# Kernel optimization log

Hardware: AMD Instinct MI355X
Metric: run time of the kernel (lower is better)

Reference implementation:

```python
import jax, jax.numpy as jnp
import numpy as np

NUM_BASES = 5
STRIDE = (1, 1)
PADDING = ((1, 1), (1, 1))
DN = ('NCHW', 'OIHW', 'NCHW')


def quantize_act(x):
    # Q_A_DOREFA forward: round(clamp(x, 0, 1)) -> values in {0, 1}
    return jnp.round(jnp.clip(x, 0.0, 1.0))


def quantize_w(w):
    # Q_W forward: sign(w) * mean(|w|) over the whole weight tensor of one basis
    return jnp.sign(w) * jnp.mean(jnp.abs(w))


def setup_inputs() -> dict:
    key = jax.random.key(0)
    kx, kw = jax.random.split(key)
    x = jax.random.normal(kx, (8, 256, 64, 64), dtype=jnp.float32)
    # 5 bases, each an OIHW conv kernel [256, 256, 3, 3]
    weights = jax.random.normal(kw, (NUM_BASES, 256, 256, 3, 3), dtype=jnp.float32) * 0.05
    return {"x": x, "weights": weights}


def reference(x, weights):
    xq = quantize_act(x)
    # quantize each basis independently (per-basis scalar scale)
    wq = jax.vmap(quantize_w)(weights)  # [5, O, I, kh, kw]
    # conv is linear in the kernel: sum of 5 convs == conv with summed kernels
    w_sum = jnp.sum(wq, axis=0)
    out = jax.lax.conv_general_dilated(
        xq, w_sum, window_strides=STRIDE, padding=PADDING,
        dimension_numbers=DN)
    return out / NUM_BASES
```

## Files before the change

kernel.cpp:

```cpp
#include <hip/hip_runtime.h>
#include <hip/hip_bf16.h>

typedef __attribute__((ext_vector_type(4))) int i32x4;

constexpr int NB = 8, CI = 256, OC = 256, HH = 64, WW = 64, HP = 66, WP = 66;
constexpr int NBASES = 5;
constexpr int WELEMS = OC * CI * 9;
constexpr int NT = 36;

__global__ void k_abs_partial(const float* __restrict__ w, float* __restrict__ part) {
    int b = blockIdx.x >> 6, chunk = blockIdx.x & 63;
    const float4* v = (const float4*)(w + (size_t)b * WELEMS + (size_t)chunk * (WELEMS / 64));
    float s = 0.f;
    for (int i = threadIdx.x; i < WELEMS / 64 / 4; i += 256) {
        float4 t = v[i];
        s += fabsf(t.x) + fabsf(t.y) + fabsf(t.z) + fabsf(t.w);
    }
    #pragma unroll
    for (int off = 32; off; off >>= 1) s += __shfl_down(s, off, 64);
    __shared__ float ls[4];
    int lane = threadIdx.x & 63, wid = threadIdx.x >> 6;
    if (lane == 0) ls[wid] = s;
    __syncthreads();
    if (threadIdx.x == 0) part[blockIdx.x] = ls[0] + ls[1] + ls[2] + ls[3];
}

__global__ void k_prep(const float* __restrict__ w, const float* __restrict__ part,
                       signed char* __restrict__ wsum8, float* __restrict__ scl,
                       const float* __restrict__ x, signed char* __restrict__ xq) {
    __shared__ float sLDS[NBASES];
    int tid = threadIdx.x;

    if (blockIdx.x < OC) {
        if (tid < 64) {
            #pragma unroll
            for (int b = 0; b < NBASES; ++b) {
                float v = part[b * 64 + tid];
                #pragma unroll
                for (int off = 32; off; off >>= 1) v += __shfl_down(v, off, 64);
                if (tid == 0) sLDS[b] = v * (1.0f / (float)WELEMS);
            }
        }
        __syncthreads();
        float sc[NBASES];
        #pragma unroll
        for (int b = 0; b < NBASES; ++b) sc[b] = sLDS[b];
        float sSum = sc[0] + sc[1] + sc[2] + sc[3] + sc[4];
        float invS = 127.0f / sSum;
        if (blockIdx.x == 0 && tid == 0)
            scl[0] = sSum * (0.2f / 127.0f);

        int o = blockIdx.x, i = tid;
        const float* base = w + ((size_t)(o * CI + i)) * 9;
        float acc[9];
        #pragma unroll
        for (int t = 0; t < 9; ++t) acc[t] = 0.f;
        #pragma unroll
        for (int b = 0; b < NBASES; ++b) {
            const float* wb = base + (size_t)b * WELEMS;
            #pragma unroll
            for (int t = 0; t < 9; ++t) {
                float xv = wb[t];
                acc[t] += (xv > 0.f) ? sc[b] : ((xv < 0.f) ? -sc[b] : 0.f);
            }
        }
        #pragma unroll
        for (int t = 0; t < 9; ++t)
            wsum8[(t * OC + o) * CI + i] = (signed char)__float2int_rn(acc[t] * invS);
        return;
    }

    int nh = blockIdx.x - OC, n = nh >> 6, h = nh & 63;
    const float* xb = x + ((size_t)n * CI) * (HH * WW) + h * WW;
    signed char* ob = xq + ((size_t)(n * HP + (h + 1)) * WP + 1) * CI;
    int w4 = tid >> 2;
    int cl = tid & 3;
    #pragma unroll
    for (int p = 0; p < 4; ++p) {
        int c = (p * 4 + cl) * 16;
        signed char pk[16];
        #pragma unroll
        for (int i = 0; i < 16; ++i) {
            float v = xb[(size_t)(c + i) * (HH * WW) + w4];
            pk[i] = (signed char)rintf(fminf(fmaxf(v, 0.f), 1.f));
        }
        *(int4*)(ob + w4 * CI + c) = *(const int4*)pk;
    }
    (ob - CI)[tid] = 0;
    (ob + 64 * CI)[tid] = 0;
    if (h == 0) {
        signed char* r0 = xq + ((size_t)(n * HP + 0) * WP) * CI;
        int4 z = {0, 0, 0, 0};
        for (int i = tid; i < WP * CI / 16; i += 256) *(int4*)(r0 + i * 16) = z;
    }
    if (h == HH - 1) {
        signed char* r65 = xq + ((size_t)(n * HP + (HP - 1)) * WP) * CI;
        int4 z = {0, 0, 0, 0};
        for (int i = tid; i < WP * CI / 16; i += 256) *(int4*)(r65 + i * 16) = z;
    }
}

__launch_bounds__(256, 2)
__global__ void k_conv(const signed char* __restrict__ xq,
                       const signed char* __restrict__ wsum,
                       const float* __restrict__ scl,
                       float* __restrict__ out) {
    __shared__ __align__(16) signed char lA[4][128 * 64];
    __shared__ __align__(16) signed char lB[4][128 * 64];

    float so = scl[0];

    int bid = blockIdx.x;
    int bx = ((bid & 7) << 6) | (bid >> 3);
    int pt = bx >> 1, ot = bx & 1;
    int pb = pt * 128;
    int n = pb >> 12;
    int h0 = (pb >> 6) & 63;
    int oc0 = ot * 128;
    int tid = threadIdx.x;

    int base0 = (n * HP + h0) * WP * CI;
    int bBase0 = oc0 * CI;

    int aOff[2], bOff[2];
    #pragma unroll
    for (int k = 0; k < 2; ++k) {
        int c = tid + k * 256;
        int row = c >> 2, sp = c & 3;
        int l = sp ^ ((row >> 1) & 3);
        aOff[k] = ((row >> 6) * WP + (row & 63)) * CI + l * 16;
        bOff[k] = row * CI + l * 16;
    }

    int lane = tid & 63, wid = tid >> 6;
    int wm = wid >> 1, wn = wid & 1;
    int g = lane >> 4, r16 = lane & 15;
    int fA[4], fB[4];
    #pragma unroll
    for (int q = 0; q < 4; ++q) {
        int ra = wm * 64 + q * 16 + r16;
        fA[q] = ra * 64 + (g ^ ((ra >> 1) & 3)) * 16;
        int rb = wn * 64 + q * 16 + r16;
        fB[q] = rb * 64 + (g ^ ((rb >> 1) & 3)) * 16;
    }

    i32x4 acc[4][4] = {};

    auto stage = [&](int t) {
        int buf = t & 3;
        int tap = t >> 2;
        int c0 = (t & 3) << 6;
        int kh = (tap * 171) >> 9;
        int kw = tap - kh * 3;
        const signed char* aSrc = xq + base0 + (kh * WP + kw) * CI + c0;
        const signed char* bSrc = wsum + tap * (OC * CI) + bBase0 + c0;
        #pragma unroll
        for (int k = 0; k < 2; ++k) {
            __builtin_amdgcn_global_load_lds(
                (const __attribute__((address_space(1))) void*)(aSrc + aOff[k]),
                (__attribute__((address_space(3))) void*)(&lA[buf][(tid + k * 256) * 16]), 16, 0, 0);
            __builtin_amdgcn_global_load_lds(
                (const __attribute__((address_space(1))) void*)(bSrc + bOff[k]),
                (__attribute__((address_space(3))) void*)(&lB[buf][(tid + k * 256) * 16]), 16, 0, 0);
        }
    };
    auto readFrags = [&](int buf, i32x4 (&aR)[4], i32x4 (&bR)[4]) {
        #pragma unroll
        for (int q = 0; q < 4; ++q) aR[q] = *(const i32x4*)&lA[buf][fA[q]];
        #pragma unroll
        for (int q = 0; q < 4; ++q) bR[q] = *(const i32x4*)&lB[buf][fB[q]];
    };
    auto mfmaCluster = [&](i32x4 (&aR)[4], i32x4 (&bR)[4]) {
        __builtin_amdgcn_s_setprio(1);
        #pragma unroll
        for (int mq = 0; mq < 4; ++mq)
            #pragma unroll
            for (int nq = 0; nq < 4; ++nq)
                acc[mq][nq] = __builtin_amdgcn_mfma_i32_16x16x64_i8(
                    aR[mq], bR[nq], acc[mq][nq], 0, 0, 0);
        __builtin_amdgcn_s_setprio(0);
    };

    stage(0); stage(1); stage(2);
    asm volatile("s_waitcnt vmcnt(8)" ::: "memory");
    __builtin_amdgcn_s_barrier();
    i32x4 a0[4], b0[4], a1[4], b1[4];
    readFrags(0, a0, b0);

    #pragma unroll 1
    for (int p = 0; p < NT / 2; ++p) {
        int t = 2 * p;
        {
            if (t + 2 <= NT - 1) asm volatile("s_waitcnt vmcnt(4)" ::: "memory");
            else                 asm volatile("s_waitcnt vmcnt(0)" ::: "memory");
            __builtin_amdgcn_s_barrier();
            __builtin_amdgcn_sched_barrier(0);
            if (t + 3 < NT) stage(t + 3);
            readFrags((t + 1) & 3, a1, b1);
            __builtin_amdgcn_sched_barrier(0);
            mfmaCluster(a0, b0);
        }
        t = 2 * p + 1;
        {
            if (t < NT - 1) {
                if (t + 2 <= NT - 1) asm volatile("s_waitcnt vmcnt(4)" ::: "memory");
                else                 asm volatile("s_waitcnt vmcnt(0)" ::: "memory");
                __builtin_amdgcn_s_barrier();
                __builtin_amdgcn_sched_barrier(0);
                if (t + 3 < NT) stage(t + 3);
                readFrags((t + 1) & 3, a0, b0);
                __builtin_amdgcn_sched_barrier(0);
            }
            mfmaCluster(a1, b1);
        }
    }

    int hw0 = pb & 4095;
    #pragma unroll
    for (int mq = 0; mq < 4; ++mq) {
        int pl = wm * 64 + mq * 16 + g * 4;
        #pragma unroll
        for (int nq = 0; nq < 4; ++nq) {
            int oc = oc0 + wn * 64 + nq * 16 + r16;
            float4 v;
            v.x = (float)acc[mq][nq][0] * so;
            v.y = (float)acc[mq][nq][1] * so;
            v.z = (float)acc[mq][nq][2] * so;
            v.w = (float)acc[mq][nq][3] * so;
            *(float4*)(out + ((size_t)(n * OC + oc) << 12) + hw0 + pl) = v;
        }
    }
}

extern "C" void kernel_launch(void* const* d_in, const int* in_sizes, int n_in,
                              void* d_out, int out_size, void* d_ws, size_t ws_size,
                              hipStream_t stream) {
    (void)in_sizes; (void)n_in; (void)out_size; (void)ws_size;
    const float* x   = (const float*)d_in[0];
    const float* wts = (const float*)d_in[1];
    float* out = (float*)d_out;
    char* wsb = (char*)d_ws;
    float* part          = (float*)wsb;
    float* scl           = (float*)(wsb + 2048);
    signed char* wsum8   = (signed char*)(wsb + 4096);
    signed char* xq8     = (signed char*)(wsb + (size_t)(2u << 20));

    hipLaunchKernelGGL(k_abs_partial, dim3(NBASES * 64), dim3(256), 0, stream, wts, part);
    hipLaunchKernelGGL(k_prep, dim3(OC + NB * HH), dim3(256), 0, stream,
                       wts, part, wsum8, scl, x, xq8);
    hipLaunchKernelGGL(k_conv, dim3((NB * HH * WW / 128) * (OC / 128)), dim3(256), 0, stream,
                       xq8, wsum8, scl, out);
}
```

Baseline: 52.75 us.

## Load activation fragments directly from global into registers, bypassing LDS

The activation (A) operand is now loaded straight from global memory into per-lane MFMA fragment registers, one tap ahead. This replaces the global-to-LDS staging plus the LDS reads used before. Only the weight (B) tiles still go through the 4-deep LDS ring, so the A shared buffer is dropped and the vmcnt waits are retuned for the new load counts. The aim is to cut LDS traffic and footprint. The cost is duplicate global reads of A across the two N-waves and more exposed global-load latency in the MFMA loop.

```diff
diff --git a/kernel.cpp b/kernel.cpp
--- a/kernel.cpp
+++ b/kernel.cpp
@@ -105,7 +105,6 @@
                        const signed char* __restrict__ wsum,
                        const float* __restrict__ scl,
                        float* __restrict__ out) {
-    __shared__ __align__(16) signed char lA[4][128 * 64];
     __shared__ __align__(16) signed char lB[4][128 * 64];
 
     float so = scl[0];
@@ -122,53 +121,60 @@
     int base0 = (n * HP + h0) * WP * CI;
     int bBase0 = oc0 * CI;
 
-    int aOff[2], bOff[2];
+    int bOff[2];
     #pragma unroll
     for (int k = 0; k < 2; ++k) {
         int c = tid + k * 256;
         int row = c >> 2, sp = c & 3;
         int l = sp ^ ((row >> 1) & 3);
-        aOff[k] = ((row >> 6) * WP + (row & 63)) * CI + l * 16;
         bOff[k] = row * CI + l * 16;
     }
 
     int lane = tid & 63, wid = tid >> 6;
     int wm = wid >> 1, wn = wid & 1;
     int g = lane >> 4, r16 = lane & 15;
-    int fA[4], fB[4];
+    int pA[4];
     #pragma unroll
     for (int q = 0; q < 4; ++q) {
         int ra = wm * 64 + q * 16 + r16;
-        fA[q] = ra * 64 + (g ^ ((ra >> 1) & 3)) * 16;
+        pA[q] = ((ra >> 6) * WP + (ra & 63)) * CI + g * 16;
+    }
+    int fB[4];
+    #pragma unroll
+    for (int q = 0; q < 4; ++q) {
         int rb = wn * 64 + q * 16 + r16;
         fB[q] = rb * 64 + (g ^ ((rb >> 1) & 3)) * 16;
     }
 
     i32x4 acc[4][4] = {};
 
-    auto stage = [&](int t) {
-        int buf = t & 3;
+    auto tapBase = [&](int t) {
         int tap = t >> 2;
         int c0 = (t & 3) << 6;
         int kh = (tap * 171) >> 9;
         int kw = tap - kh * 3;
-        const signed char* aSrc = xq + base0 + (kh * WP + kw) * CI + c0;
+        return base0 + (kh * WP + kw) * CI + c0;
+    };
+    auto loadA = [&](int t, i32x4 (&aR)[4]) {
+        const signed char* s = xq + tapBase(t);
+        #pragma unroll
+        for (int q = 0; q < 4; ++q) aR[q] = *(const i32x4*)(s + pA[q]);
+    };
+    auto stageB = [&](int t) {
+        int buf = t & 3;
+        int tap = t >> 2;
+        int c0 = (t & 3) << 6;
         const signed char* bSrc = wsum + tap * (OC * CI) + bBase0 + c0;
         #pragma unroll
-        for (int k = 0; k < 2; ++k) {
-            __builtin_amdgcn_global_load_lds(
-                (const __attribute__((address_space(1))) void*)(aSrc + aOff[k]),
-                (__attribute__((address_space(3))) void*)(&lA[buf][(tid + k * 256) * 16]), 16, 0, 0);
+        for (int k = 0; k < 2; ++k)
             __builtin_amdgcn_global_load_lds(
                 (const __attribute__((address_space(1))) void*)(bSrc + bOff[k]),
                 (__attribute__((address_space(3))) void*)(&lB[buf][(tid + k * 256) * 16]), 16, 0, 0);
-        }
-    };
-    auto readFrags = [&](int buf, i32x4 (&aR)[4], i32x4 (&bR)[4]) {
-        #pragma unroll
-        for (int q = 0; q < 4; ++q) aR[q] = *(const i32x4*)&lA[buf][fA[q]];
-        #pragma unroll
-        for (int q = 0; q < 4; ++q) bR[q] = *(const i32x4*)&lB[buf][fB[q]];
+    };
+    auto readB = [&](int t, i32x4 (&bR)[4]) {
+        const signed char* B = &lB[t & 3][0];
+        #pragma unroll
+        for (int q = 0; q < 4; ++q) bR[q] = *(const i32x4*)(B + fB[q]);
     };
     auto mfmaCluster = [&](i32x4 (&aR)[4], i32x4 (&bR)[4]) {
         __builtin_amdgcn_s_setprio(1);
@@ -181,37 +187,37 @@
         __builtin_amdgcn_s_setprio(0);
     };
 
-    stage(0); stage(1); stage(2);
-    asm volatile("s_waitcnt vmcnt(8)" ::: "memory");
-    __builtin_amdgcn_s_barrier();
-    i32x4 a0[4], b0[4], a1[4], b1[4];
-    readFrags(0, a0, b0);
+    i32x4 aA[4], aB[4], bA[4], bB[4];
+
+    loadA(0, aA);
+    stageB(0); stageB(1); stageB(2);
 
     #pragma unroll 1
     for (int p = 0; p < NT / 2; ++p) {
-        int t = 2 * p;
         {
-            if (t + 2 <= NT - 1) asm volatile("s_waitcnt vmcnt(4)" ::: "memory");
-            else                 asm volatile("s_waitcnt vmcnt(0)" ::: "memory");
+            int t = 2 * p;
+            if (t <= 33) asm volatile("s_waitcnt vmcnt(2)" ::: "memory");
+            else         asm volatile("s_waitcnt vmcnt(0)" ::: "memory");
             __builtin_amdgcn_s_barrier();
             __builtin_amdgcn_sched_barrier(0);
-            if (t + 3 < NT) stage(t + 3);
-            readFrags((t + 1) & 3, a1, b1);
-            __builtin_amdgcn_sched_barrier(0);
-            mfmaCluster(a0, b0);
-        }
-        t = 2 * p + 1;
+            if (t == 0) readB(0, bA);
+            if (t + 1 < NT) loadA(t + 1, aB);
+            if (t + 3 < NT) stageB(t + 3);
+            if (t + 1 < NT) readB(t + 1, bB);
+            __builtin_amdgcn_sched_barrier(0);
+            mfmaCluster(aA, bA);
+        }
         {
-            if (t < NT - 1) {
-                if (t + 2 <= NT - 1) asm volatile("s_waitcnt vmcnt(4)" ::: "memory");
-                else                 asm volatile("s_waitcnt vmcnt(0)" ::: "memory");
-                __builtin_amdgcn_s_barrier();
-                __builtin_amdgcn_sched_barrier(0);
-                if (t + 3 < NT) stage(t + 3);
-                readFrags((t + 1) & 3, a0, b0);
-                __builtin_amdgcn_sched_barrier(0);
-            }
-            mfmaCluster(a1, b1);
+            int t = 2 * p + 1;
+            if (t <= 33) asm volatile("s_waitcnt vmcnt(2)" ::: "memory");
+            else         asm volatile("s_waitcnt vmcnt(0)" ::: "memory");
+            __builtin_amdgcn_s_barrier();
+            __builtin_amdgcn_sched_barrier(0);
+            if (t + 1 < NT) loadA(t + 1, aA);
+            if (t + 3 < NT) stageB(t + 3);
+            if (t + 1 < NT) readB(t + 1, bA);
+            __builtin_amdgcn_sched_barrier(0);
+            mfmaCluster(aB, bB);
         }
     }
 
```

Result: slower. 67.17 us (+27.3%).

## Pack weight sign bits during abs-sum pass and build summed kernel from bitmasks

Applied to the files above, without the earlier changes.

The abs-mean reduction kernel now also writes one sign bit per weight into a packed bitmask buffer. The prep kernel builds the summed int8 kernel from those bits and a 32-entry lookup table of scale combinations. This replaces its second full read of the five float weight tensors with a read about 32x smaller, and removes its strided per-thread float loads. The cost is an extra bitmask write in the first kernel. A weight of exactly zero is now treated as positive, where sign() would give zero.

```diff
diff --git a/kernel.cpp b/kernel.cpp
--- a/kernel.cpp
+++ b/kernel.cpp
@@ -7,14 +7,28 @@
 constexpr int NBASES = 5;
 constexpr int WELEMS = OC * CI * 9;
 constexpr int NT = 36;
-
-__global__ void k_abs_partial(const float* __restrict__ w, float* __restrict__ part) {
-    int b = blockIdx.x >> 6, chunk = blockIdx.x & 63;
-    const float4* v = (const float4*)(w + (size_t)b * WELEMS + (size_t)chunk * (WELEMS / 64));
+constexpr int ABS_CHUNK = 8192;
+constexpr int SIGN_BYTES = WELEMS / 8;
+
+__global__ void k_abs_partial(const float* __restrict__ w, float* __restrict__ part,
+                              unsigned char* __restrict__ signs) {
+    int b = blockIdx.x / 72, chunk = blockIdx.x % 72;
+    const float* wb = w + (size_t)b * WELEMS + chunk * ABS_CHUNK;
+    unsigned char* sb = signs + (size_t)b * SIGN_BYTES + chunk * (ABS_CHUNK / 8);
     float s = 0.f;
-    for (int i = threadIdx.x; i < WELEMS / 64 / 4; i += 256) {
-        float4 t = v[i];
-        s += fabsf(t.x) + fabsf(t.y) + fabsf(t.z) + fabsf(t.w);
+    #pragma unroll
+    for (int j = 0; j < 4; ++j) {
+        int byteIdx = threadIdx.x + j * 256;
+        float4 v0 = *(const float4*)(wb + byteIdx * 8);
+        float4 v1 = *(const float4*)(wb + byteIdx * 8 + 4);
+        s += fabsf(v0.x) + fabsf(v0.y) + fabsf(v0.z) + fabsf(v0.w)
+           + fabsf(v1.x) + fabsf(v1.y) + fabsf(v1.z) + fabsf(v1.w);
+        unsigned m = 0;
+        m |= (v0.x < 0.f) ? 1u   : 0u;  m |= (v0.y < 0.f) ? 2u   : 0u;
+        m |= (v0.z < 0.f) ? 4u   : 0u;  m |= (v0.w < 0.f) ? 8u   : 0u;
+        m |= (v1.x < 0.f) ? 16u  : 0u;  m |= (v1.y < 0.f) ? 32u  : 0u;
+        m |= (v1.z < 0.f) ? 64u  : 0u;  m |= (v1.w < 0.f) ? 128u : 0u;
+        sb[byteIdx] = (unsigned char)m;
     }
     #pragma unroll
     for (int off = 32; off; off >>= 1) s += __shfl_down(s, off, 64);
@@ -25,17 +39,19 @@
     if (threadIdx.x == 0) part[blockIdx.x] = ls[0] + ls[1] + ls[2] + ls[3];
 }
 
-__global__ void k_prep(const float* __restrict__ w, const float* __restrict__ part,
+__global__ void k_prep(const unsigned char* __restrict__ signs,
+                       const float* __restrict__ part,
                        signed char* __restrict__ wsum8, float* __restrict__ scl,
                        const float* __restrict__ x, signed char* __restrict__ xq) {
     __shared__ float sLDS[NBASES];
+    __shared__ float lutq[32];
     int tid = threadIdx.x;
 
     if (blockIdx.x < OC) {
         if (tid < 64) {
             #pragma unroll
             for (int b = 0; b < NBASES; ++b) {
-                float v = part[b * 64 + tid];
+                float v = part[b * 72 + tid] + (tid < 8 ? part[b * 72 + 64 + tid] : 0.f);
                 #pragma unroll
                 for (int off = 32; off; off >>= 1) v += __shfl_down(v, off, 64);
                 if (tid == 0) sLDS[b] = v * (1.0f / (float)WELEMS);
@@ -49,24 +65,33 @@
         float invS = 127.0f / sSum;
         if (blockIdx.x == 0 && tid == 0)
             scl[0] = sSum * (0.2f / 127.0f);
+        if (tid < 32) {
+            float a = 0.f;
+            #pragma unroll
+            for (int b = 0; b < NBASES; ++b)
+                a += ((tid >> b) & 1) ? -sc[b] : sc[b];
+            lutq[tid] = a * invS;
+        }
+        __syncthreads();
 
         int o = blockIdx.x, i = tid;
-        const float* base = w + ((size_t)(o * CI + i)) * 9;
-        float acc[9];
-        #pragma unroll
-        for (int t = 0; t < 9; ++t) acc[t] = 0.f;
+        int e0 = (o * CI + i) * 9;
+        int bytePos = e0 >> 3, shift = e0 & 7;
+        unsigned bits[NBASES];
         #pragma unroll
         for (int b = 0; b < NBASES; ++b) {
-            const float* wb = base + (size_t)b * WELEMS;
-            #pragma unroll
-            for (int t = 0; t < 9; ++t) {
-                float xv = wb[t];
-                acc[t] += (xv > 0.f) ? sc[b] : ((xv < 0.f) ? -sc[b] : 0.f);
-            }
-        }
-        #pragma unroll
-        for (int t = 0; t < 9; ++t)
-            wsum8[(t * OC + o) * CI + i] = (signed char)__float2int_rn(acc[t] * invS);
+            const unsigned char* sb = signs + (size_t)b * SIGN_BYTES + bytePos;
+            unsigned v = (unsigned)sb[0] | ((unsigned)sb[1] << 8);
+            bits[b] = (v >> shift) & 0x1FFu;
+        }
+        #pragma unroll
+        for (int t = 0; t < 9; ++t) {
+            unsigned mask = 0;
+            #pragma unroll
+            for (int b = 0; b < NBASES; ++b)
+                mask |= ((bits[b] >> t) & 1u) << b;
+            wsum8[(t * OC + o) * CI + i] = (signed char)__float2int_rn(lutq[mask]);
+        }
         return;
     }
 
@@ -243,11 +268,13 @@
     float* part          = (float*)wsb;
     float* scl           = (float*)(wsb + 2048);
     signed char* wsum8   = (signed char*)(wsb + 4096);
+    unsigned char* signs = (unsigned char*)(wsb + (size_t)(1u << 20));
     signed char* xq8     = (signed char*)(wsb + (size_t)(2u << 20));
 
-    hipLaunchKernelGGL(k_abs_partial, dim3(NBASES * 64), dim3(256), 0, stream, wts, part);
+    hipLaunchKernelGGL(k_abs_partial, dim3(NBASES * 72), dim3(256), 0, stream,
+                       wts, part, signs);
     hipLaunchKernelGGL(k_prep, dim3(OC + NB * HH), dim3(256), 0, stream,
-                       wts, part, wsum8, scl, x, xq8);
+                       signs, part, wsum8, scl, x, xq8);
     hipLaunchKernelGGL(k_conv, dim3((NB * HH * WW / 128) * (OC / 128)), dim3(256), 0, stream,
                        xq8, wsum8, scl, out);
 }
```

Result: faster. 47.41 us, median of 2 (-10.1%).
